# Kernel tuning notes

Measured on AMD Instinct MI355X. Metric: run time of the kernel, lower is better.

The kernel has to match this reference:

```python
import jax, jax.numpy as jnp
import numpy as np

N_NODES = 100000
N_EDGES = 3200000
IN_DIM, HID_DIM, OUT_DIM = 128, 64, 2


def setup_inputs() -> dict:
    key = jax.random.key(0)
    k1, k2, k3, k4 = jax.random.split(key, 4)
    x = jax.random.normal(k1, (N_NODES, IN_DIM), dtype=jnp.float32)
    edge_index = jax.random.randint(k2, (2, N_EDGES), 0, N_NODES, dtype=jnp.int64)
    # GCNConv weights (glorot-style scale) and zero biases
    W1 = jax.random.normal(k3, (IN_DIM, HID_DIM), dtype=jnp.float32) / np.sqrt(IN_DIM)
    b1 = jnp.zeros((HID_DIM,), dtype=jnp.float32)
    W2 = jax.random.normal(k4, (HID_DIM, OUT_DIM), dtype=jnp.float32) / np.sqrt(HID_DIM)
    b2 = jnp.zeros((OUT_DIM,), dtype=jnp.float32)
    return {"x": x, "edge_index": edge_index, "W1": W1, "b1": b1, "W2": W2, "b2": b2}


def _gcn_norm(edge_index, num_nodes):
    # PyG GCNConv default: add self-loops, symmetric normalization deg^-1/2.
    loops = jnp.arange(num_nodes, dtype=edge_index.dtype)
    src = jnp.concatenate([edge_index[0], loops])  # [E+N]
    dst = jnp.concatenate([edge_index[1], loops])  # [E+N]
    deg = jax.ops.segment_sum(jnp.ones_like(dst, dtype=jnp.float32), dst,
                              num_segments=num_nodes)  # in-degree incl. self-loop
    dinv = jnp.where(deg > 0, jax.lax.rsqrt(deg), 0.0)
    norm = dinv[src] * dinv[dst]  # [E+N]
    return src, dst, norm


def _gcn_conv(h, W, b, src, dst, norm, num_nodes):
    h = h @ W                              # dense transform first (smaller dim)
    msg = h[src] * norm[:, None]           # gather + scale: [E+N, d]
    out = jax.ops.segment_sum(msg, dst, num_segments=num_nodes)  # scatter-add
    return out + b


def reference(x, edge_index, W1, b1, W2, b2):
    n = x.shape[0]
    src, dst, norm = _gcn_norm(edge_index, n)
    h = _gcn_conv(x, W1, b1, src, dst, norm, n)
    h = jax.nn.relu(h)
    return _gcn_conv(h, W2, b2, src, dst, norm, n)
```

## Files before the change

### kernel.cpp

```cpp
#include <hip/hip_runtime.h>
#include <hip/hip_bf16.h>


#define N_NODES 100000
#define IN_DIM 128
#define HID_DIM 64
#define OUT_DIM 2
#define NB 391
#define BCAP 12288
#define CROUNDS 12
#define CHUNK 8192

typedef short bf16x8 __attribute__((ext_vector_type(8)));
typedef float f32x4 __attribute__((ext_vector_type(4)));

__device__ __forceinline__ unsigned short f2bf(float x) {
    unsigned int u = __float_as_uint(x);
    unsigned int r = (u + 0x7FFFu + ((u >> 16) & 1u)) >> 16;
    return (unsigned short)r;
}
__device__ __forceinline__ float bflo(unsigned int u) { return __uint_as_float(u << 16); }
__device__ __forceinline__ float bfhi(unsigned int u) { return __uint_as_float(u & 0xFFFF0000u); }
__device__ __forceinline__ float4 unplo(uint4 r) {
    return make_float4(bflo(r.x), bflo(r.y), bflo(r.z), bflo(r.w));
}
__device__ __forceinline__ float4 unphi(uint4 r) {
    return make_float4(bfhi(r.x), bfhi(r.y), bfhi(r.z), bfhi(r.w));
}
__device__ __forceinline__ float4 f4add(float4 a, float4 v) {
    return make_float4(a.x + v.x, a.y + v.y, a.z + v.z, a.w + v.w);
}
__device__ __forceinline__ float4 f4fma(float m, float4 v, float4 a) {
    return make_float4(fmaf(m, v.x, a.x), fmaf(m, v.y, a.y),
                       fmaf(m, v.z, a.z), fmaf(m, v.w, a.w));
}
__device__ __forceinline__ int wave_incl_scan(int v, int laneid) {
#pragma unroll
    for (int off = 1; off < 64; off <<= 1) {
        int u = __shfl_up(v, off);
        if (laneid >= off) v += u;
    }
    return v;
}

__global__ __launch_bounds__(512) void part_kernel(const int* __restrict__ ei,
                                                   int* __restrict__ gCursor,
                                                   int* __restrict__ part, int E) {
    __shared__ int hist[512], lrow[512], gbase[512], lcur[512];
    __shared__ int lpk[CHUNK];
    __shared__ short lbkt[CHUNK];
    __shared__ int wsum[8], wofs[8];
    const int t = threadIdx.x;
    const int lane = t & 63, wv = t >> 6;
    const int base = blockIdx.x * CHUNK;
    const int cntC = min(CHUNK, E - base);

    hist[t] = 0;
    __syncthreads();

    int s[16], d[16];
    bool val[16];
    if (base + CHUNK <= E) {
#pragma unroll
        for (int i = 0; i < 4; ++i) {
            int4 sv = ((const int4*)(ei + base))[t + i * 512];
            int4 dv = ((const int4*)(ei + E + base))[t + i * 512];
            s[i * 4 + 0] = sv.x; s[i * 4 + 1] = sv.y; s[i * 4 + 2] = sv.z; s[i * 4 + 3] = sv.w;
            d[i * 4 + 0] = dv.x; d[i * 4 + 1] = dv.y; d[i * 4 + 2] = dv.z; d[i * 4 + 3] = dv.w;
            val[i * 4 + 0] = val[i * 4 + 1] = val[i * 4 + 2] = val[i * 4 + 3] = true;
        }
    } else {
#pragma unroll
        for (int i = 0; i < 16; ++i) {
            int e = base + t + i * 512;
            val[i] = (e < E);
            if (val[i]) {
                s[i] = ei[e];
                d[i] = ei[E + e];
            }
        }
    }
#pragma unroll
    for (int i = 0; i < 16; ++i)
        if (val[i]) atomicAdd(&hist[d[i] >> 8], 1);
    __syncthreads();

    int v = hist[t];
    int inc = wave_incl_scan(v, lane);
    if (lane == 63) wsum[wv] = inc;
    __syncthreads();
    if (t < 64) {
        int w = (t < 8) ? wsum[t] : 0;
        int wi = wave_incl_scan(w, t);
        if (t < 8) wofs[t] = wi - w;
    }
    __syncthreads();
    int excl = inc - v + wofs[wv];
    if (t < NB && v > 0) {
        int old = atomicAdd(&gCursor[t], v);
        gbase[t] = t * BCAP + old;
    }
    lcur[t] = excl;
    lrow[t] = excl;
    __syncthreads();

#pragma unroll
    for (int i = 0; i < 16; ++i) {
        if (val[i]) {
            int b = d[i] >> 8;
            int pos = atomicAdd(&lcur[b], 1);
            lpk[pos] = s[i] | ((d[i] & 255) << 20);
            lbkt[pos] = (short)b;
        }
    }
    __syncthreads();

    for (int i = t; i < cntC; i += 512) {
        int b = lbkt[i];
        int g = gbase[b] + (i - lrow[b]);
        if (g < (b + 1) * BCAP)
            part[g] = lpk[i];
    }
}

__global__ __launch_bounds__(1024) void csr_kernel(const int* __restrict__ part,
                                                   const int* __restrict__ gCursor,
                                                   int* __restrict__ cnt,
                                                   float* __restrict__ dinv,
                                                   int* __restrict__ rowptr,
                                                   int* __restrict__ csr_src, int n) {
    __shared__ int wcnt[16][256];
    __shared__ int wsum[4], wofs[4];
    const int b = blockIdx.x, t = threadIdx.x;
    const int lane = t & 63, wv = t >> 6;
    const int start = b * BCAP;
    const int count = min(gCursor[b], BCAP);

    for (int i = t; i < 16 * 256; i += 1024) ((int*)wcnt)[i] = 0;
    __syncthreads();

    int pk[CROUNDS];
    bool val[CROUNDS];
#pragma unroll
    for (int k = 0; k < CROUNDS; ++k) {
        int i = t + k * 1024;
        val[k] = (i < count);
        pk[k] = val[k] ? part[start + i] : 0;
        if (val[k]) atomicAdd(&wcnt[wv][(pk[k] >> 20) & 255], 1);
    }
    __syncthreads();

    int v = 0;
    if (t < 256) {
        int sum = 0;
#pragma unroll
        for (int w = 0; w < 16; ++w) sum += wcnt[w][t];
        v = sum;
    }
    int inc = 0;
    if (t < 256) {
        inc = wave_incl_scan(v, lane);
        if (lane == 63) wsum[wv] = inc;
    }
    __syncthreads();
    if (t < 64) {
        int w = (t < 4) ? wsum[t] : 0;
        int wi = wave_incl_scan(w, t);
        if (t < 4) wofs[t] = wi - w;
    }
    __syncthreads();
    if (t < 256) {
        int excl = inc - v + wofs[wv];
        int node = (b << 8) + t;
        if (node < n) {
            cnt[node] = v;
            dinv[node] = rsqrtf((float)v + 1.0f);
            rowptr[node] = start + excl;
        }
        int run = excl;
#pragma unroll
        for (int w = 0; w < 16; ++w) {
            int c = wcnt[w][t];
            wcnt[w][t] = run;
            run += c;
        }
    }
    __syncthreads();

#pragma unroll
    for (int k = 0; k < CROUNDS; ++k) {
        if (val[k]) {
            int pos = atomicAdd(&wcnt[wv][(pk[k] >> 20) & 255], 1);
            csr_src[start + pos] = pk[k] & 0xFFFFF;
        }
    }
}

__global__ __launch_bounds__(256) void gemm1_kernel(const float* __restrict__ x,
                                                    const float* __restrict__ W1,
                                                    const float* __restrict__ dinv,
                                                    unsigned short* __restrict__ hsb, int n) {
    __shared__ unsigned short sX[64 * 136];
    __shared__ unsigned short sW[64 * 136];
    const int tid = threadIdx.x;
    const int rbase = blockIdx.x * 64;

    for (int i = tid; i < 2048; i += 256) {
        int k = i >> 4, cq = (i & 15) << 2;
        float4 v = ((const float4*)W1)[i];
        sW[(cq + 0) * 136 + k] = f2bf(v.x);
        sW[(cq + 1) * 136 + k] = f2bf(v.y);
        sW[(cq + 2) * 136 + k] = f2bf(v.z);
        sW[(cq + 3) * 136 + k] = f2bf(v.w);
    }
    for (int i = tid; i < 2048; i += 256) {
        int r = i >> 5, kq = (i & 31) << 2;
        int gr = rbase + r;
        float4 v = make_float4(0.f, 0.f, 0.f, 0.f);
        if (gr < n) v = ((const float4*)x)[gr * 32 + (i & 31)];
        ushort4 u;
        u.x = f2bf(v.x); u.y = f2bf(v.y); u.z = f2bf(v.z); u.w = f2bf(v.w);
        *(ushort4*)&sX[r * 136 + kq] = u;
    }
    __syncthreads();

    const int wave = tid >> 6, lane = tid & 63;
    const int quad = lane >> 4, l16 = lane & 15;
    const int rowoff = wave * 16;

    f32x4 acc[4];
#pragma unroll
    for (int t = 0; t < 4; ++t) acc[t] = (f32x4){0.f, 0.f, 0.f, 0.f};

#pragma unroll
    for (int k0 = 0; k0 < 128; k0 += 32) {
        bf16x8 a = *(const bf16x8*)&sX[(rowoff + l16) * 136 + k0 + quad * 8];
#pragma unroll
        for (int t = 0; t < 4; ++t) {
            bf16x8 b = *(const bf16x8*)&sW[(t * 16 + l16) * 136 + k0 + quad * 8];
            acc[t] = __builtin_amdgcn_mfma_f32_16x16x32_bf16(a, b, acc[t], 0, 0, 0);
        }
    }

#pragma unroll
    for (int r = 0; r < 4; ++r) {
        int grow = rbase + rowoff + quad * 4 + r;
        if (grow < n) {
            float di = dinv[grow];
#pragma unroll
            for (int t = 0; t < 4; ++t)
                hsb[grow * HID_DIM + t * 16 + l16] = f2bf(acc[t][r] * di);
        }
    }
}

__global__ __launch_bounds__(256) void agg1_kernel(const int* __restrict__ rowptr,
                                                   const int* __restrict__ cnt,
                                                   const int* __restrict__ csr_src,
                                                   const unsigned short* __restrict__ hsb,
                                                   const float* __restrict__ dinv,
                                                   const float* __restrict__ b1,
                                                   const float* __restrict__ W2,
                                                   float* __restrict__ hs2, int n) {
    int node = blockIdx.x * 4 + (threadIdx.x >> 6);
    if (node >= n) return;
    int lane = threadIdx.x & 63;
    int g = lane >> 3;
    int l = lane & 7;
    int start = rowptr[node];
    int deg = cnt[node];

    float4 alo = make_float4(0.f, 0.f, 0.f, 0.f);
    float4 ahi = make_float4(0.f, 0.f, 0.f, 0.f);
    int s0 = (g      < deg) ? csr_src[start + g]      : 0;
    int s1 = (g +  8 < deg) ? csr_src[start + g +  8] : 0;
    int s2 = (g + 16 < deg) ? csr_src[start + g + 16] : 0;
    int s3 = (g + 24 < deg) ? csr_src[start + g + 24] : 0;
    for (int j = g; j < deg; j += 32) {
        int p0 = (j + 32 < deg) ? csr_src[start + j + 32] : 0;
        int p1 = (j + 40 < deg) ? csr_src[start + j + 40] : 0;
        int p2 = (j + 48 < deg) ? csr_src[start + j + 48] : 0;
        int p3 = (j + 56 < deg) ? csr_src[start + j + 56] : 0;
        uint4 r0 = *(const uint4*)&hsb[(unsigned)s0 * HID_DIM + l * 8];
        uint4 r1 = *(const uint4*)&hsb[(unsigned)s1 * HID_DIM + l * 8];
        uint4 r2 = *(const uint4*)&hsb[(unsigned)s2 * HID_DIM + l * 8];
        uint4 r3 = *(const uint4*)&hsb[(unsigned)s3 * HID_DIM + l * 8];
        float m1 = (j +  8 < deg) ? 1.0f : 0.0f;
        float m2 = (j + 16 < deg) ? 1.0f : 0.0f;
        float m3 = (j + 24 < deg) ? 1.0f : 0.0f;
        alo = f4add(alo, unplo(r0));      ahi = f4add(ahi, unphi(r0));
        alo = f4fma(m1, unplo(r1), alo);  ahi = f4fma(m1, unphi(r1), ahi);
        alo = f4fma(m2, unplo(r2), alo);  ahi = f4fma(m2, unphi(r2), ahi);
        alo = f4fma(m3, unplo(r3), alo);  ahi = f4fma(m3, unphi(r3), ahi);
        s0 = p0; s1 = p1; s2 = p2; s3 = p3;
    }

    float a[8];
    a[0] = alo.x; a[1] = ahi.x; a[2] = alo.y; a[3] = ahi.y;
    a[4] = alo.z; a[5] = ahi.z; a[6] = alo.w; a[7] = ahi.w;

#pragma unroll
    for (int off = 8; off <= 32; off <<= 1) {
#pragma unroll
        for (int i = 0; i < 8; ++i) a[i] += __shfl_xor(a[i], off);
    }

    {
        uint4 raw = *(const uint4*)&hsb[(unsigned)node * HID_DIM + l * 8];
        a[0] += bflo(raw.x); a[1] += bfhi(raw.x);
        a[2] += bflo(raw.y); a[3] += bfhi(raw.y);
        a[4] += bflo(raw.z); a[5] += bfhi(raw.z);
        a[6] += bflo(raw.w); a[7] += bfhi(raw.w);
    }

    float di = dinv[node];
    float4 bb0 = *(const float4*)&b1[l * 8];
    float4 bb1 = *(const float4*)&b1[l * 8 + 4];
    float t0 = fmaxf(fmaf(di, a[0], bb0.x), 0.0f);
    float t1 = fmaxf(fmaf(di, a[1], bb0.y), 0.0f);
    float t2 = fmaxf(fmaf(di, a[2], bb0.z), 0.0f);
    float t3 = fmaxf(fmaf(di, a[3], bb0.w), 0.0f);
    float t4 = fmaxf(fmaf(di, a[4], bb1.x), 0.0f);
    float t5 = fmaxf(fmaf(di, a[5], bb1.y), 0.0f);
    float t6 = fmaxf(fmaf(di, a[6], bb1.z), 0.0f);
    float t7 = fmaxf(fmaf(di, a[7], bb1.w), 0.0f);

    float4 w0 = *(const float4*)&W2[l * 16];
    float4 w1 = *(const float4*)&W2[l * 16 + 4];
    float4 w2 = *(const float4*)&W2[l * 16 + 8];
    float4 w3 = *(const float4*)&W2[l * 16 + 12];
    float p0 = t0 * w0.x + t1 * w0.z + t2 * w1.x + t3 * w1.z
             + t4 * w2.x + t5 * w2.z + t6 * w3.x + t7 * w3.z;
    float p1 = t0 * w0.y + t1 * w0.w + t2 * w1.y + t3 * w1.w
             + t4 * w2.y + t5 * w2.w + t6 * w3.y + t7 * w3.w;
    p0 += __shfl_xor(p0, 1);  p1 += __shfl_xor(p1, 1);
    p0 += __shfl_xor(p0, 2);  p1 += __shfl_xor(p1, 2);
    p0 += __shfl_xor(p0, 4);  p1 += __shfl_xor(p1, 4);

    if (lane == 0) {
        hs2[node * OUT_DIM + 0] = di * p0;
        hs2[node * OUT_DIM + 1] = di * p1;
    }
}

__global__ __launch_bounds__(256) void agg2_kernel(const int* __restrict__ rowptr,
                                                   const int* __restrict__ cnt,
                                                   const int* __restrict__ csr_src,
                                                   const float* __restrict__ hs2,
                                                   const float* __restrict__ dinv,
                                                   const float* __restrict__ b2,
                                                   float* __restrict__ out, int n) {
    int node = blockIdx.x * 8 + (threadIdx.x >> 5);
    if (node >= n) return;
    int lane = threadIdx.x & 31;
    int start = rowptr[node];
    int deg = cnt[node];

    float a0 = 0.0f, a1 = 0.0f;
    for (int j = lane; j < deg; j += 32) {
        int s = csr_src[start + j];
        float2 v = *(const float2*)&hs2[s * OUT_DIM];
        a0 += v.x;
        a1 += v.y;
    }
#pragma unroll
    for (int off = 16; off > 0; off >>= 1) {
        a0 += __shfl_xor(a0, off);
        a1 += __shfl_xor(a1, off);
    }
    if (lane == 0) {
        float di = dinv[node];
        float2 self = *(const float2*)&hs2[node * OUT_DIM];
        out[node * OUT_DIM + 0] = di * (a0 + self.x) + b2[0];
        out[node * OUT_DIM + 1] = di * (a1 + self.y) + b2[1];
    }
}

extern "C" void kernel_launch(void* const* d_in, const int* in_sizes, int n_in,
                              void* d_out, int out_size, void* d_ws, size_t ws_size,
                              hipStream_t stream) {
    const float* x  = (const float*)d_in[0];
    const int*   ei = (const int*)d_in[1];
    const float* W1 = (const float*)d_in[2];
    const float* b1 = (const float*)d_in[3];
    const float* W2 = (const float*)d_in[4];
    const float* b2 = (const float*)d_in[5];
    float* out = (float*)d_out;

    const int n = N_NODES;
    const int E = in_sizes[1] / 2;

    char* ws = (char*)d_ws;
    int*   gCursor = (int*)  (ws + 0);
    int*   cnt     = (int*)  (ws + (1u << 20));
    float* dinv    = (float*)(ws + (2u << 20));
    int*   rowptr  = (int*)  (ws + (3u << 20));
    float* hs2     = (float*)(ws + (4u << 20));
    int*   part    = (int*)  (ws + (5u << 20));
    unsigned short* hsb = (unsigned short*)(ws + (5u << 20));
    int*   csr_src = (int*)  (ws + (25u << 20));

    hipMemsetAsync(gCursor, 0, NB * sizeof(int), stream);

    part_kernel<<<(E + CHUNK - 1) / CHUNK, 512, 0, stream>>>(ei, gCursor, part, E);
    csr_kernel<<<NB, 1024, 0, stream>>>(part, gCursor, cnt, dinv, rowptr, csr_src, n);

    gemm1_kernel<<<(n + 63) / 64, 256, 0, stream>>>(x, W1, dinv, hsb, n);
    agg1_kernel<<<(n + 3) / 4, 256, 0, stream>>>(rowptr, cnt, csr_src, hsb, dinv, b1, W2, hs2, n);
    agg2_kernel<<<(n + 7) / 8, 256, 0, stream>>>(rowptr, cnt, csr_src, hs2, dinv, b2, out, n);
}
```

Baseline: 240.9 us.

## Shrink agg1 to 16 lanes per node with int4 index loads and zero-row padding

Result: faster. 235.6 us (-2.2%).

```diff
diff --git a/kernel.cpp b/kernel.cpp
--- a/kernel.cpp
+++ b/kernel.cpp
@@ -10,6 +10,7 @@
 #define BCAP 12288
 #define CROUNDS 12
 #define CHUNK 8192
+#define ZROW N_NODES
 
 typedef short bf16x8 __attribute__((ext_vector_type(8)));
 typedef float f32x4 __attribute__((ext_vector_type(4)));
@@ -21,18 +22,11 @@
 }
 __device__ __forceinline__ float bflo(unsigned int u) { return __uint_as_float(u << 16); }
 __device__ __forceinline__ float bfhi(unsigned int u) { return __uint_as_float(u & 0xFFFF0000u); }
-__device__ __forceinline__ float4 unplo(uint4 r) {
-    return make_float4(bflo(r.x), bflo(r.y), bflo(r.z), bflo(r.w));
-}
-__device__ __forceinline__ float4 unphi(uint4 r) {
-    return make_float4(bfhi(r.x), bfhi(r.y), bfhi(r.z), bfhi(r.w));
-}
-__device__ __forceinline__ float4 f4add(float4 a, float4 v) {
-    return make_float4(a.x + v.x, a.y + v.y, a.z + v.z, a.w + v.w);
-}
-__device__ __forceinline__ float4 f4fma(float m, float4 v, float4 a) {
-    return make_float4(fmaf(m, v.x, a.x), fmaf(m, v.y, a.y),
-                       fmaf(m, v.z, a.z), fmaf(m, v.w, a.w));
+__device__ __forceinline__ f32x4 vlo(uint4 r) {
+    return (f32x4){bflo(r.x), bflo(r.y), bflo(r.z), bflo(r.w)};
+}
+__device__ __forceinline__ f32x4 vhi(uint4 r) {
+    return (f32x4){bfhi(r.x), bfhi(r.y), bfhi(r.z), bfhi(r.w)};
 }
 __device__ __forceinline__ int wave_incl_scan(int v, int laneid) {
 #pragma unroll
@@ -150,16 +144,17 @@
     }
     __syncthreads();
 
-    int v = 0;
+    int v = 0, pv = 0;
     if (t < 256) {
         int sum = 0;
 #pragma unroll
         for (int w = 0; w < 16; ++w) sum += wcnt[w][t];
         v = sum;
+        pv = (v + 3) & ~3;
     }
     int inc = 0;
     if (t < 256) {
-        inc = wave_incl_scan(v, lane);
+        inc = wave_incl_scan(pv, lane);
         if (lane == 63) wsum[wv] = inc;
     }
     __syncthreads();
@@ -170,7 +165,7 @@
     }
     __syncthreads();
     if (t < 256) {
-        int excl = inc - v + wofs[wv];
+        int excl = inc - pv + wofs[wv];
         int node = (b << 8) + t;
         if (node < n) {
             cnt[node] = v;
@@ -262,51 +257,50 @@
                                                    const float* __restrict__ b1,
                                                    const float* __restrict__ W2,
                                                    float* __restrict__ hs2, int n) {
-    int node = blockIdx.x * 4 + (threadIdx.x >> 6);
-    if (node >= n) return;
-    int lane = threadIdx.x & 63;
-    int g = lane >> 3;
-    int l = lane & 7;
-    int start = rowptr[node];
-    int deg = cnt[node];
-
-    float4 alo = make_float4(0.f, 0.f, 0.f, 0.f);
-    float4 ahi = make_float4(0.f, 0.f, 0.f, 0.f);
-    int s0 = (g      < deg) ? csr_src[start + g]      : 0;
-    int s1 = (g +  8 < deg) ? csr_src[start + g +  8] : 0;
-    int s2 = (g + 16 < deg) ? csr_src[start + g + 16] : 0;
-    int s3 = (g + 24 < deg) ? csr_src[start + g + 24] : 0;
-    for (int j = g; j < deg; j += 32) {
-        int p0 = (j + 32 < deg) ? csr_src[start + j + 32] : 0;
-        int p1 = (j + 40 < deg) ? csr_src[start + j + 40] : 0;
-        int p2 = (j + 48 < deg) ? csr_src[start + j + 48] : 0;
-        int p3 = (j + 56 < deg) ? csr_src[start + j + 56] : 0;
-        uint4 r0 = *(const uint4*)&hsb[(unsigned)s0 * HID_DIM + l * 8];
-        uint4 r1 = *(const uint4*)&hsb[(unsigned)s1 * HID_DIM + l * 8];
-        uint4 r2 = *(const uint4*)&hsb[(unsigned)s2 * HID_DIM + l * 8];
-        uint4 r3 = *(const uint4*)&hsb[(unsigned)s3 * HID_DIM + l * 8];
-        float m1 = (j +  8 < deg) ? 1.0f : 0.0f;
-        float m2 = (j + 16 < deg) ? 1.0f : 0.0f;
-        float m3 = (j + 24 < deg) ? 1.0f : 0.0f;
-        alo = f4add(alo, unplo(r0));      ahi = f4add(ahi, unphi(r0));
-        alo = f4fma(m1, unplo(r1), alo);  ahi = f4fma(m1, unphi(r1), ahi);
-        alo = f4fma(m2, unplo(r2), alo);  ahi = f4fma(m2, unphi(r2), ahi);
-        alo = f4fma(m3, unplo(r3), alo);  ahi = f4fma(m3, unphi(r3), ahi);
-        s0 = p0; s1 = p1; s2 = p2; s3 = p3;
+    const int node = blockIdx.x * 16 + (threadIdx.x >> 4);
+    const int lane16 = threadIdx.x & 15;
+    const int g = lane16 >> 3;
+    const int l = lane16 & 7;
+    const int start = rowptr[node];
+    const int deg = cnt[node];
+    const unsigned lofs = (unsigned)l * 8;
+
+    f32x4 alo = (f32x4){0.f, 0.f, 0.f, 0.f};
+    f32x4 ahi = (f32x4){0.f, 0.f, 0.f, 0.f};
+
+    const int4* qp = (const int4*)csr_src + (start >> 2) + g;
+    int4 cur = qp[0];
+    int q = 0;
+    for (;;) {
+        const int e = q * 8 + 4 * g;
+        const bool pf = (e + 8 < deg);
+        int4 nxt = pf ? qp[2 * q + 2] : make_int4(ZROW, ZROW, ZROW, ZROW);
+        int s0 = (e + 0 < deg) ? cur.x : ZROW;
+        int s1 = (e + 1 < deg) ? cur.y : ZROW;
+        int s2 = (e + 2 < deg) ? cur.z : ZROW;
+        int s3 = (e + 3 < deg) ? cur.w : ZROW;
+        uint4 r0 = *(const uint4*)&hsb[(unsigned)s0 * HID_DIM + lofs];
+        uint4 r1 = *(const uint4*)&hsb[(unsigned)s1 * HID_DIM + lofs];
+        uint4 r2 = *(const uint4*)&hsb[(unsigned)s2 * HID_DIM + lofs];
+        uint4 r3 = *(const uint4*)&hsb[(unsigned)s3 * HID_DIM + lofs];
+        alo += vlo(r0);  ahi += vhi(r0);
+        alo += vlo(r1);  ahi += vhi(r1);
+        alo += vlo(r2);  ahi += vhi(r2);
+        alo += vlo(r3);  ahi += vhi(r3);
+        cur = nxt;
+        ++q;
+        if (q * 8 >= deg) break;
     }
 
     float a[8];
-    a[0] = alo.x; a[1] = ahi.x; a[2] = alo.y; a[3] = ahi.y;
-    a[4] = alo.z; a[5] = ahi.z; a[6] = alo.w; a[7] = ahi.w;
-
-#pragma unroll
-    for (int off = 8; off <= 32; off <<= 1) {
-#pragma unroll
-        for (int i = 0; i < 8; ++i) a[i] += __shfl_xor(a[i], off);
-    }
+    a[0] = alo[0]; a[1] = ahi[0]; a[2] = alo[1]; a[3] = ahi[1];
+    a[4] = alo[2]; a[5] = ahi[2]; a[6] = alo[3]; a[7] = ahi[3];
+
+#pragma unroll
+    for (int i = 0; i < 8; ++i) a[i] += __shfl_xor(a[i], 8);
 
     {
-        uint4 raw = *(const uint4*)&hsb[(unsigned)node * HID_DIM + l * 8];
+        uint4 raw = *(const uint4*)&hsb[(unsigned)node * HID_DIM + lofs];
         a[0] += bflo(raw.x); a[1] += bfhi(raw.x);
         a[2] += bflo(raw.y); a[3] += bfhi(raw.y);
         a[4] += bflo(raw.z); a[5] += bfhi(raw.z);
@@ -337,9 +331,8 @@
     p0 += __shfl_xor(p0, 2);  p1 += __shfl_xor(p1, 2);
     p0 += __shfl_xor(p0, 4);  p1 += __shfl_xor(p1, 4);
 
-    if (lane == 0) {
-        hs2[node * OUT_DIM + 0] = di * p0;
-        hs2[node * OUT_DIM + 1] = di * p1;
+    if (lane16 == 0) {
+        *(float2*)&hs2[node * OUT_DIM] = make_float2(di * p0, di * p1);
     }
 }
 
@@ -405,7 +398,10 @@
     part_kernel<<<(E + CHUNK - 1) / CHUNK, 512, 0, stream>>>(ei, gCursor, part, E);
     csr_kernel<<<NB, 1024, 0, stream>>>(part, gCursor, cnt, dinv, rowptr, csr_src, n);
 
+    hipMemsetAsync(hsb + (size_t)N_NODES * HID_DIM, 0,
+                   HID_DIM * sizeof(unsigned short), stream);
+
     gemm1_kernel<<<(n + 63) / 64, 256, 0, stream>>>(x, W1, dinv, hsb, n);
-    agg1_kernel<<<(n + 3) / 4, 256, 0, stream>>>(rowptr, cnt, csr_src, hsb, dinv, b1, W2, hs2, n);
+    agg1_kernel<<<n / 16, 256, 0, stream>>>(rowptr, cnt, csr_src, hsb, dinv, b1, W2, hs2, n);
     agg2_kernel<<<(n + 7) / 8, 256, 0, stream>>>(rowptr, cnt, csr_src, hs2, dinv, b2, out, n);
 }
```
